# Optimization experiments

Measured on AMD Instinct MI355X. Metric: run time of the kernel, lower is better.

Reference implementation:

```python
import jax, jax.numpy as jnp
import numpy as np

N_NODES = 50000
N_EDGES = 800000


def setup_inputs() -> dict:
    key = jax.random.key(0)
    ks = jax.random.split(key, 8)
    x = jax.random.normal(ks[0], (N_NODES, 128), dtype=jnp.float32)
    edge_index = jax.random.randint(ks[1], (2, N_EDGES), 0, N_NODES, dtype=jnp.int64)
    # Glorot-ish scaled weights (GCNConv uses glorot init)
    W1 = jax.random.normal(ks[2], (128, 128), dtype=jnp.float32) * 0.08
    W2 = jax.random.normal(ks[3], (128, 128), dtype=jnp.float32) * 0.08
    W3 = jax.random.normal(ks[4], (128, 64), dtype=jnp.float32) * 0.08
    b1 = jnp.zeros((128,), jnp.float32)
    b2 = jnp.zeros((128,), jnp.float32)
    b3 = jnp.zeros((64,), jnp.float32)
    return {"x": x, "W1": W1, "b1": b1, "W2": W2, "b2": b2,
            "W3": W3, "b3": b3, "edge_index": edge_index}


def _gcn_layer(x, W, b, src, dst, norm, n):
    # GCNConv: out = D^{-1/2} (A+I) D^{-1/2} (x W) + b
    h = x @ W                                   # [N, F_out]
    msg = h[src] * norm[:, None]                # gather + scale per edge
    agg = jax.ops.segment_sum(msg, dst, num_segments=n)  # scatter-add
    return agg + b


def reference(x, W1, b1, W2, b2, W3, b3, edge_index):
    n = x.shape[0]
    loops = jnp.arange(n, dtype=edge_index.dtype)
    src = jnp.concatenate([edge_index[0], loops])  # add self-loops (PyG default)
    dst = jnp.concatenate([edge_index[1], loops])
    # symmetric normalization from in-degree (incl. self-loops)
    deg = jax.ops.segment_sum(jnp.ones_like(dst, dtype=x.dtype), dst, num_segments=n)
    dis = jnp.where(deg > 0, jax.lax.rsqrt(deg), 0.0)
    norm = dis[src] * dis[dst]                   # [E+N]

    h = jax.nn.relu(_gcn_layer(x, W1, b1, src, dst, norm, n))
    # dropout(p=0.5) is identity in eval mode
    h = jax.nn.relu(_gcn_layer(h, W2, b2, src, dst, norm, n))
    h = _gcn_layer(h, W3, b3, src, dst, norm, n)
    return jax.nn.log_softmax(h, axis=1)
```

## Files before the change

kernel.cpp:

```cpp
#include <hip/hip_runtime.h>
#include <hip/hip_bf16.h>
#include <cstdint>

typedef unsigned int uint32;
typedef unsigned short ushort;
typedef __attribute__((ext_vector_type(8))) short short8;
typedef __attribute__((ext_vector_type(4))) float f32x4;

#define EPB 4096
#define CAP 8192

__device__ inline ushort bf16r(float f) {
    uint32 u = __float_as_uint(f);
    u += 0x7fff + ((u >> 16) & 1);
    return (ushort)(u >> 16);
}
__device__ inline uint32 pack_bf16(float a, float b) {
    return (uint32)bf16r(a) | ((uint32)bf16r(b) << 16);
}
__device__ inline float bf_lo(uint32 w) { return __uint_as_float(w << 16); }
__device__ inline float bf_hi(uint32 w) { return __uint_as_float(w & 0xffff0000u); }


__global__ __launch_bounds__(256) void k_part_prep(
        const int* __restrict__ srcv, const int* __restrict__ dstv,
        int* __restrict__ bcnt, uint64_t* __restrict__ pairs, int e, int nbE,
        const float* __restrict__ W1, const float* __restrict__ W2, const float* __restrict__ W3,
        ushort* __restrict__ Wt1, ushort* __restrict__ Wt2, ushort* __restrict__ Wt3) {
    int bid = blockIdx.x, t = threadIdx.x;
    if (bid >= nbE) {
        int wb = bid - nbE;
        const float* W = wb == 0 ? W1 : (wb == 1 ? W2 : W3);
        ushort* Wt = wb == 0 ? Wt1 : (wb == 1 ? Wt2 : Wt3);
        int F = wb == 2 ? 64 : 128;
        for (int i = t; i < 128 * F; i += 256) {
            int k = i / F, c = i % F;
            Wt[c * 128 + k] = bf16r(W[i]);
        }
        return;
    }
    __shared__ int h[256], base[256], cur[256];
    h[t] = 0; cur[t] = 0;
    __syncthreads();
    int s[EPB / 256], d[EPB / 256];
    int b0 = bid * EPB;
#pragma unroll
    for (int i = 0; i < EPB / 256; ++i) {
        int idx = b0 + i * 256 + t;
        if (idx < e) {
            s[i] = srcv[idx]; d[i] = dstv[idx];
            atomicAdd(&h[d[i] >> 8], 1);
        } else d[i] = -1;
    }
    __syncthreads();
    base[t] = h[t] ? atomicAdd(&bcnt[t], h[t]) : 0;
    __syncthreads();
#pragma unroll
    for (int i = 0; i < EPB / 256; ++i) {
        if (d[i] >= 0) {
            int b = d[i] >> 8;
            int sl = base[b] + atomicAdd(&cur[b], 1);
            if (sl < CAP) {
                uint64_t pk = (uint64_t)(unsigned)s[i] | ((uint64_t)(unsigned)d[i] << 32);
                pairs[(size_t)b * CAP + sl] = pk;
            }
        }
    }
}


__global__ __launch_bounds__(256) void k_bfinish(const uint64_t* __restrict__ pairs,
                                                 const int* __restrict__ bcnt,
                                                 int2* __restrict__ rps, float* __restrict__ dis,
                                                 int* __restrict__ col, int n) {
    __shared__ int c[256], sc[256], cur[256];
    int t = threadIdx.x;
    c[t] = 0; cur[t] = 0;
    __syncthreads();
    int wb = blockIdx.x << 8;
    int e0 = blockIdx.x * CAP;
    int e1 = e0 + min(bcnt[blockIdx.x], CAP);
    for (int i = e0 + t; i < e1; i += 256)
        atomicAdd(&c[(int)(pairs[i] >> 32) - wb], 1);
    __syncthreads();
    int own = c[t];
    sc[t] = own;
    __syncthreads();
    for (int off = 1; off < 256; off <<= 1) {
        int a = (t >= off) ? sc[t - off] : 0;
        __syncthreads();
        sc[t] += a;
        __syncthreads();
    }
    int start = blockIdx.x * CAP + sc[t] - own;
    __syncthreads();
    sc[t] = start;
    int v = wb + t;
    if (v < n) {
        rps[v] = make_int2(start, start + own);
        dis[v] = rsqrtf((float)(own + 1));
    }
    __syncthreads();
    for (int i = e0 + t; i < e1; i += 256) {
        uint64_t p = pairs[i];
        int bl = (int)(p >> 32) - wb;
        int sl = atomicAdd(&cur[bl], 1);
        col[sc[bl] + sl] = (int)(uint32)p;
    }
}


template <int FOUT, bool BF16IN>
__global__ __launch_bounds__(256) void k_gemm_mfma(
        const void* __restrict__ Xv, const ushort* __restrict__ Wt,
        const float* __restrict__ dis, ushort* __restrict__ Yb, int n) {
    constexpr int CT = FOUT / 16;
    int lane = threadIdx.x & 63;
    int wv = threadIdx.x >> 6;
    int r16 = lane & 15, kg = lane >> 4;
    int rowA = blockIdx.x * 64 + wv * 16 + r16;
    int ra = min(rowA, n - 1);
    short8 afr[4];
    if (BF16IN) {
        const ushort* Xb = (const ushort*)Xv;
#pragma unroll
        for (int ks = 0; ks < 4; ++ks)
            afr[ks] = *(const short8*)(Xb + (size_t)ra * 128 + ks * 32 + kg * 8);
    } else {
        const float* Xf = (const float*)Xv;
#pragma unroll
        for (int ks = 0; ks < 4; ++ks) {
            const float* p = Xf + (size_t)ra * 128 + ks * 32 + kg * 8;
            float4 f0 = *(const float4*)p;
            float4 f1 = *(const float4*)(p + 4);
            short8 a;
            a[0] = (short)bf16r(f0.x); a[1] = (short)bf16r(f0.y);
            a[2] = (short)bf16r(f0.z); a[3] = (short)bf16r(f0.w);
            a[4] = (short)bf16r(f1.x); a[5] = (short)bf16r(f1.y);
            a[6] = (short)bf16r(f1.z); a[7] = (short)bf16r(f1.w);
            afr[ks] = a;
        }
    }
    f32x4 acc[CT];
#pragma unroll
    for (int c = 0; c < CT; ++c) acc[c] = (f32x4){0.f, 0.f, 0.f, 0.f};
#pragma unroll
    for (int ks = 0; ks < 4; ++ks) {
#pragma unroll
        for (int c = 0; c < CT; ++c) {
            short8 b = *(const short8*)(Wt + (c * 16 + r16) * 128 + ks * 32 + kg * 8);
            acc[c] = __builtin_amdgcn_mfma_f32_16x16x32_bf16(afr[ks], b, acc[c], 0, 0, 0);
        }
    }
    int rbase = blockIdx.x * 64 + wv * 16 + kg * 4;
#pragma unroll
    for (int j = 0; j < 4; ++j) {
        int row = rbase + j;
        if (row < n) {
            float d = dis[row];
#pragma unroll
            for (int c = 0; c < CT; ++c)
                Yb[(size_t)row * FOUT + c * 16 + r16] = bf16r(acc[c][j] * d);
        }
    }
}


__global__ __launch_bounds__(256) void k_agg_relu128(
        const uint32* __restrict__ hb, const int2* __restrict__ rps,
        const int* __restrict__ col, const float* __restrict__ dis,
        const float* __restrict__ bias, uint32* __restrict__ outb, int n) {
    int wid = threadIdx.x >> 6;
    int lane = threadIdx.x & 63;
    int v = blockIdx.x * 4 + wid;
    if (v >= n) return;
    uint32 mv = hb[(size_t)v * 64 + lane];
    float ax = bf_lo(mv), ay = bf_hi(mv);
    int2 se = rps[v];
    int s = __builtin_amdgcn_readfirstlane(se.x);
    int e = __builtin_amdgcn_readfirstlane(se.y);
    int k = s;
    for (; k + 16 <= e; k += 16) {
        uint32 m[16];
#pragma unroll
        for (int j = 0; j < 16; ++j) {
            int u = col[k + j];
            m[j] = hb[(size_t)u * 64 + lane];
        }
#pragma unroll
        for (int j = 0; j < 16; ++j) { ax += bf_lo(m[j]); ay += bf_hi(m[j]); }
    }
    if (k + 8 <= e) {
        uint32 m[8];
#pragma unroll
        for (int j = 0; j < 8; ++j) m[j] = hb[(size_t)col[k + j] * 64 + lane];
#pragma unroll
        for (int j = 0; j < 8; ++j) { ax += bf_lo(m[j]); ay += bf_hi(m[j]); }
        k += 8;
    }
    if (k + 4 <= e) {
        uint32 m[4];
#pragma unroll
        for (int j = 0; j < 4; ++j) m[j] = hb[(size_t)col[k + j] * 64 + lane];
#pragma unroll
        for (int j = 0; j < 4; ++j) { ax += bf_lo(m[j]); ay += bf_hi(m[j]); }
        k += 4;
    }
    for (; k < e; ++k) {
        uint32 m = hb[(size_t)col[k] * 64 + lane];
        ax += bf_lo(m); ay += bf_hi(m);
    }
    float d = dis[v];
    float2 b = ((const float2*)bias)[lane];
    float ox = fmaxf(d * ax + b.x, 0.f);
    float oy = fmaxf(d * ay + b.y, 0.f);
    __builtin_nontemporal_store(pack_bf16(ox, oy), &outb[(size_t)v * 64 + lane]);
}

__global__ __launch_bounds__(256) void k_agg_lsm64(
        const ushort* __restrict__ hb, const int2* __restrict__ rps,
        const int* __restrict__ col, const float* __restrict__ dis,
        const float* __restrict__ bias, float* __restrict__ out, int n) {
    int wid = threadIdx.x >> 6;
    int lane = threadIdx.x & 63;
    int v = blockIdx.x * 4 + wid;
    if (v >= n) return;
    float acc = __uint_as_float((uint32)hb[(size_t)v * 64 + lane] << 16);
    int2 se = rps[v];
    int s = __builtin_amdgcn_readfirstlane(se.x);
    int e = __builtin_amdgcn_readfirstlane(se.y);
    int k = s;
    for (; k + 16 <= e; k += 16) {
        ushort m[16];
#pragma unroll
        for (int j = 0; j < 16; ++j) m[j] = hb[(size_t)col[k + j] * 64 + lane];
#pragma unroll
        for (int j = 0; j < 16; ++j) acc += __uint_as_float((uint32)m[j] << 16);
    }
    if (k + 8 <= e) {
        ushort m[8];
#pragma unroll
        for (int j = 0; j < 8; ++j) m[j] = hb[(size_t)col[k + j] * 64 + lane];
#pragma unroll
        for (int j = 0; j < 8; ++j) acc += __uint_as_float((uint32)m[j] << 16);
        k += 8;
    }
    for (; k < e; ++k) acc += __uint_as_float((uint32)hb[(size_t)col[k] * 64 + lane] << 16);
    float val = dis[v] * acc + bias[lane];
    float m = val;
    for (int off = 32; off; off >>= 1) m = fmaxf(m, __shfl_xor(m, off, 64));
    float ex = expf(val - m);
    float ss = ex;
    for (int off = 32; off; off >>= 1) ss += __shfl_xor(ss, off, 64);
    __builtin_nontemporal_store(val - m - logf(ss), &out[(size_t)v * 64 + lane]);
}


extern "C" void kernel_launch(void* const* d_in, const int* in_sizes, int n_in,
                              void* d_out, int out_size, void* d_ws, size_t ws_size,
                              hipStream_t stream) {
    const float* x  = (const float*)d_in[0];
    const float* W1 = (const float*)d_in[1];
    const float* b1 = (const float*)d_in[2];
    const float* W2 = (const float*)d_in[3];
    const float* b2 = (const float*)d_in[4];
    const float* W3 = (const float*)d_in[5];
    const float* b3 = (const float*)d_in[6];
    const int*   ei = (const int*)d_in[7];

    const int N = in_sizes[0] / 128;
    const int E = in_sizes[7] / 2;
    const int* srcv = ei;
    const int* dstv = ei + E;
    const int NB  = (N + 255) >> 8;
    const int nbE = (E + EPB - 1) / EPB;

    char* ws = (char*)d_ws;
    size_t off = 0;
    auto alloc = [&](size_t bytes) -> void* {
        void* p = ws + off;
        off += (bytes + 255) & ~(size_t)255;
        return p;
    };
    float*    dis   = (float*)alloc((size_t)N * 4);
    int2*     rps   = (int2*)alloc((size_t)N * 8);
    int*      bcnt  = (int*)alloc((size_t)NB * 4);
    int*      col   = (int*)alloc((size_t)NB * CAP * 4);
    uint64_t* pairs = (uint64_t*)alloc((size_t)NB * CAP * 8);
    ushort*   Wt1   = (ushort*)alloc(128 * 128 * 2);
    ushort*   Wt2   = (ushort*)alloc(128 * 128 * 2);
    ushort*   Wt3   = (ushort*)alloc(64 * 128 * 2);
    ushort*   hsb   = (ushort*)alloc((size_t)N * 128 * 2);
    ushort*   hbX   = (ushort*)alloc((size_t)N * 128 * 2);
    ushort*   hs3   = (ushort*)alloc((size_t)N * 64 * 2);
    float*    outp  = (float*)d_out;

    (void)hipMemsetAsync(bcnt, 0, (size_t)NB * 4, stream);
    k_part_prep<<<nbE + 3, 256, 0, stream>>>(srcv, dstv, bcnt, pairs, E, nbE,
                                             W1, W2, W3, Wt1, Wt2, Wt3);
    k_bfinish<<<NB, 256, 0, stream>>>(pairs, bcnt, rps, dis, col, N);

    int gblk = (N + 63) / 64;
    int ablk = (N + 3) / 4;
    k_gemm_mfma<128, false><<<gblk, 256, 0, stream>>>(x, Wt1, dis, hsb, N);
    k_agg_relu128<<<ablk, 256, 0, stream>>>((const uint32*)hsb, rps, col, dis, b1, (uint32*)hbX, N);
    k_gemm_mfma<128, true><<<gblk, 256, 0, stream>>>(hbX, Wt2, dis, hsb, N);
    k_agg_relu128<<<ablk, 256, 0, stream>>>((const uint32*)hsb, rps, col, dis, b2, (uint32*)hbX, N);
    k_gemm_mfma<64, true><<<gblk, 256, 0, stream>>>(hbX, Wt3, dis, hs3, N);
    k_agg_lsm64<<<ablk, 256, 0, stream>>>(hs3, rps, col, dis, b3, outp, N);
}
```

Measured before the change: 186.0 us.

## Split 128-wide hidden features into two 64-column planes aggregated separately

Hidden feature matrices are stored as two planes of 64 bf16 columns each, and the 128-wide aggregation runs as two passes, one per plane. Each pass gathers 128-byte rows instead of 256-byte rows, so a plane's working set (about 6.4 MB) is more likely to stay in L2/MALL cache during the random neighbor gathers. In exchange the edge list and column indices are read twice, there are extra kernel launches, and each lane now does 16-bit loads.

```diff
diff --git a/kernel.cpp b/kernel.cpp
--- a/kernel.cpp
+++ b/kernel.cpp
@@ -15,11 +15,7 @@
     u += 0x7fff + ((u >> 16) & 1);
     return (ushort)(u >> 16);
 }
-__device__ inline uint32 pack_bf16(float a, float b) {
-    return (uint32)bf16r(a) | ((uint32)bf16r(b) << 16);
-}
-__device__ inline float bf_lo(uint32 w) { return __uint_as_float(w << 16); }
-__device__ inline float bf_hi(uint32 w) { return __uint_as_float(w & 0xffff0000u); }
+__device__ inline float bfu(ushort w) { return __uint_as_float((uint32)w << 16); }
 
 
 __global__ __launch_bounds__(256) void k_part_prep(
@@ -60,10 +56,9 @@
         if (d[i] >= 0) {
             int b = d[i] >> 8;
             int sl = base[b] + atomicAdd(&cur[b], 1);
-            if (sl < CAP) {
-                uint64_t pk = (uint64_t)(unsigned)s[i] | ((uint64_t)(unsigned)d[i] << 32);
-                pairs[(size_t)b * CAP + sl] = pk;
-            }
+            if (sl < CAP)
+                pairs[(size_t)b * CAP + sl] =
+                    (uint64_t)(unsigned)s[i] | ((uint64_t)(unsigned)d[i] << 32);
         }
     }
 }
@@ -110,10 +105,10 @@
 }
 
 
-template <int FOUT, bool BF16IN>
+template <int FOUT, int INMODE>
 __global__ __launch_bounds__(256) void k_gemm_mfma(
         const void* __restrict__ Xv, const ushort* __restrict__ Wt,
-        const float* __restrict__ dis, ushort* __restrict__ Yb, int n) {
+        const float* __restrict__ dis, ushort* __restrict__ Yb, int n, size_t plsz) {
     constexpr int CT = FOUT / 16;
     int lane = threadIdx.x & 63;
     int wv = threadIdx.x >> 6;
@@ -121,11 +116,12 @@
     int rowA = blockIdx.x * 64 + wv * 16 + r16;
     int ra = min(rowA, n - 1);
     short8 afr[4];
-    if (BF16IN) {
+    if (INMODE == 1) {
         const ushort* Xb = (const ushort*)Xv;
 #pragma unroll
         for (int ks = 0; ks < 4; ++ks)
-            afr[ks] = *(const short8*)(Xb + (size_t)ra * 128 + ks * 32 + kg * 8);
+            afr[ks] = *(const short8*)(Xb + (size_t)(ks >> 1) * plsz +
+                                       (size_t)ra * 64 + (ks & 1) * 32 + kg * 8);
     } else {
         const float* Xf = (const float*)Xv;
 #pragma unroll
@@ -159,62 +155,57 @@
         if (row < n) {
             float d = dis[row];
 #pragma unroll
-            for (int c = 0; c < CT; ++c)
-                Yb[(size_t)row * FOUT + c * 16 + r16] = bf16r(acc[c][j] * d);
-        }
-    }
-}
-
-
-__global__ __launch_bounds__(256) void k_agg_relu128(
-        const uint32* __restrict__ hb, const int2* __restrict__ rps,
+            for (int c = 0; c < CT; ++c) {
+                ushort val = bf16r(acc[c][j] * d);
+                if (FOUT == 128)
+                    Yb[(size_t)(c >> 2) * plsz + (size_t)row * 64 + (c & 3) * 16 + r16] = val;
+                else
+                    Yb[(size_t)row * 64 + c * 16 + r16] = val;
+            }
+        }
+    }
+}
+
+
+__global__ __launch_bounds__(256) void k_agg_plane(
+        const ushort* __restrict__ hp, const int2* __restrict__ rps,
         const int* __restrict__ col, const float* __restrict__ dis,
-        const float* __restrict__ bias, uint32* __restrict__ outb, int n) {
+        const float* __restrict__ bias, ushort* __restrict__ outp, int n) {
     int wid = threadIdx.x >> 6;
     int lane = threadIdx.x & 63;
     int v = blockIdx.x * 4 + wid;
     if (v >= n) return;
-    uint32 mv = hb[(size_t)v * 64 + lane];
-    float ax = bf_lo(mv), ay = bf_hi(mv);
+    float ax = bfu(hp[(size_t)v * 64 + lane]);
     int2 se = rps[v];
     int s = __builtin_amdgcn_readfirstlane(se.x);
     int e = __builtin_amdgcn_readfirstlane(se.y);
     int k = s;
     for (; k + 16 <= e; k += 16) {
-        uint32 m[16];
-#pragma unroll
-        for (int j = 0; j < 16; ++j) {
-            int u = col[k + j];
-            m[j] = hb[(size_t)u * 64 + lane];
-        }
-#pragma unroll
-        for (int j = 0; j < 16; ++j) { ax += bf_lo(m[j]); ay += bf_hi(m[j]); }
+        ushort m[16];
+#pragma unroll
+        for (int j = 0; j < 16; ++j) m[j] = hp[(size_t)col[k + j] * 64 + lane];
+#pragma unroll
+        for (int j = 0; j < 16; ++j) ax += bfu(m[j]);
     }
     if (k + 8 <= e) {
-        uint32 m[8];
-#pragma unroll
-        for (int j = 0; j < 8; ++j) m[j] = hb[(size_t)col[k + j] * 64 + lane];
-#pragma unroll
-        for (int j = 0; j < 8; ++j) { ax += bf_lo(m[j]); ay += bf_hi(m[j]); }
+        ushort m[8];
+#pragma unroll
+        for (int j = 0; j < 8; ++j) m[j] = hp[(size_t)col[k + j] * 64 + lane];
+#pragma unroll
+        for (int j = 0; j < 8; ++j) ax += bfu(m[j]);
         k += 8;
     }
     if (k + 4 <= e) {
-        uint32 m[4];
-#pragma unroll
-        for (int j = 0; j < 4; ++j) m[j] = hb[(size_t)col[k + j] * 64 + lane];
-#pragma unroll
-        for (int j = 0; j < 4; ++j) { ax += bf_lo(m[j]); ay += bf_hi(m[j]); }
+        ushort m[4];
+#pragma unroll
+        for (int j = 0; j < 4; ++j) m[j] = hp[(size_t)col[k + j] * 64 + lane];
+#pragma unroll
+        for (int j = 0; j < 4; ++j) ax += bfu(m[j]);
         k += 4;
     }
-    for (; k < e; ++k) {
-        uint32 m = hb[(size_t)col[k] * 64 + lane];
-        ax += bf_lo(m); ay += bf_hi(m);
-    }
-    float d = dis[v];
-    float2 b = ((const float2*)bias)[lane];
-    float ox = fmaxf(d * ax + b.x, 0.f);
-    float oy = fmaxf(d * ay + b.y, 0.f);
-    __builtin_nontemporal_store(pack_bf16(ox, oy), &outb[(size_t)v * 64 + lane]);
+    for (; k < e; ++k) ax += bfu(hp[(size_t)col[k] * 64 + lane]);
+    float ox = fmaxf(dis[v] * ax + bias[lane], 0.f);
+    __builtin_nontemporal_store(bf16r(ox), &outp[(size_t)v * 64 + lane]);
 }
 
 __global__ __launch_bounds__(256) void k_agg_lsm64(
@@ -225,7 +216,7 @@
     int lane = threadIdx.x & 63;
     int v = blockIdx.x * 4 + wid;
     if (v >= n) return;
-    float acc = __uint_as_float((uint32)hb[(size_t)v * 64 + lane] << 16);
+    float acc = bfu(hb[(size_t)v * 64 + lane]);
     int2 se = rps[v];
     int s = __builtin_amdgcn_readfirstlane(se.x);
     int e = __builtin_amdgcn_readfirstlane(se.y);
@@ -235,17 +226,17 @@
 #pragma unroll
         for (int j = 0; j < 16; ++j) m[j] = hb[(size_t)col[k + j] * 64 + lane];
 #pragma unroll
-        for (int j = 0; j < 16; ++j) acc += __uint_as_float((uint32)m[j] << 16);
+        for (int j = 0; j < 16; ++j) acc += bfu(m[j]);
     }
     if (k + 8 <= e) {
         ushort m[8];
 #pragma unroll
         for (int j = 0; j < 8; ++j) m[j] = hb[(size_t)col[k + j] * 64 + lane];
 #pragma unroll
-        for (int j = 0; j < 8; ++j) acc += __uint_as_float((uint32)m[j] << 16);
+        for (int j = 0; j < 8; ++j) acc += bfu(m[j]);
         k += 8;
     }
-    for (; k < e; ++k) acc += __uint_as_float((uint32)hb[(size_t)col[k] * 64 + lane] << 16);
+    for (; k < e; ++k) acc += bfu(hb[(size_t)col[k] * 64 + lane]);
     float val = dis[v] * acc + bias[lane];
     float m = val;
     for (int off = 32; off; off >>= 1) m = fmaxf(m, __shfl_xor(m, off, 64));
@@ -274,6 +265,7 @@
     const int* dstv = ei + E;
     const int NB  = (N + 255) >> 8;
     const int nbE = (E + EPB - 1) / EPB;
+    const size_t PLSZ = (size_t)N * 64;
 
     char* ws = (char*)d_ws;
     size_t off = 0;
@@ -290,9 +282,9 @@
     ushort*   Wt1   = (ushort*)alloc(128 * 128 * 2);
     ushort*   Wt2   = (ushort*)alloc(128 * 128 * 2);
     ushort*   Wt3   = (ushort*)alloc(64 * 128 * 2);
-    ushort*   hsb   = (ushort*)alloc((size_t)N * 128 * 2);
-    ushort*   hbX   = (ushort*)alloc((size_t)N * 128 * 2);
-    ushort*   hs3   = (ushort*)alloc((size_t)N * 64 * 2);
+    ushort*   hsA   = (ushort*)alloc(PLSZ * 2 * 2);
+    ushort*   hbB   = (ushort*)alloc(PLSZ * 2 * 2);
+    ushort*   hs3   = (ushort*)alloc(PLSZ * 2);
     float*    outp  = (float*)d_out;
 
     (void)hipMemsetAsync(bcnt, 0, (size_t)NB * 4, stream);
@@ -302,10 +294,12 @@
 
     int gblk = (N + 63) / 64;
     int ablk = (N + 3) / 4;
-    k_gemm_mfma<128, false><<<gblk, 256, 0, stream>>>(x, Wt1, dis, hsb, N);
-    k_agg_relu128<<<ablk, 256, 0, stream>>>((const uint32*)hsb, rps, col, dis, b1, (uint32*)hbX, N);
-    k_gemm_mfma<128, true><<<gblk, 256, 0, stream>>>(hbX, Wt2, dis, hsb, N);
-    k_agg_relu128<<<ablk, 256, 0, stream>>>((const uint32*)hsb, rps, col, dis, b2, (uint32*)hbX, N);
-    k_gemm_mfma<64, true><<<gblk, 256, 0, stream>>>(hbX, Wt3, dis, hs3, N);
+    k_gemm_mfma<128, 0><<<gblk, 256, 0, stream>>>(x, Wt1, dis, hsA, N, PLSZ);
+    k_agg_plane<<<ablk, 256, 0, stream>>>(hsA,        rps, col, dis, b1,      hbB,        N);
+    k_agg_plane<<<ablk, 256, 0, stream>>>(hsA + PLSZ, rps, col, dis, b1 + 64, hbB + PLSZ, N);
+    k_gemm_mfma<128, 1><<<gblk, 256, 0, stream>>>(hbB, Wt2, dis, hsA, N, PLSZ);
+    k_agg_plane<<<ablk, 256, 0, stream>>>(hsA,        rps, col, dis, b2,      hbB,        N);
+    k_agg_plane<<<ablk, 256, 0, stream>>>(hsA + PLSZ, rps, col, dis, b2 + 64, hbB + PLSZ, N);
+    k_gemm_mfma<64, 1><<<gblk, 256, 0, stream>>>(hbB, Wt3, dis, hs3, N, PLSZ);
     k_agg_lsm64<<<ablk, 256, 0, stream>>>(hs3, rps, col, dis, b3, outp, N);
 }
```

New measurement: 211.1 us. 1.14x slower.

## Split wavefront into sub-groups gathering multiple edges with wider loads

Applied to the files above, without the earlier changes.

The aggregation kernels now split each 64-lane wavefront into 2 groups (128-feature layer) or 4 groups (64-feature layer). Each group processes a different neighbor at the same time and every lane loads 8 bytes instead of 4 or 2. Partial sums are combined with cross-lane shuffles, and the self-loop term and bias are added at the end. This puts more independent row gathers in flight per instruction and widens the memory accesses. The cost is extra shuffles, masked tail iterations, and only half or a quarter of the lanes doing the final stores.

```diff
diff --git a/kernel.cpp b/kernel.cpp
--- a/kernel.cpp
+++ b/kernel.cpp
@@ -60,10 +60,9 @@
         if (d[i] >= 0) {
             int b = d[i] >> 8;
             int sl = base[b] + atomicAdd(&cur[b], 1);
-            if (sl < CAP) {
-                uint64_t pk = (uint64_t)(unsigned)s[i] | ((uint64_t)(unsigned)d[i] << 32);
-                pairs[(size_t)b * CAP + sl] = pk;
-            }
+            if (sl < CAP)
+                pairs[(size_t)b * CAP + sl] =
+                    (uint64_t)(unsigned)s[i] | ((uint64_t)(unsigned)d[i] << 32);
         }
     }
 }
@@ -172,87 +171,137 @@
         const float* __restrict__ bias, uint32* __restrict__ outb, int n) {
     int wid = threadIdx.x >> 6;
     int lane = threadIdx.x & 63;
+    int grp = lane >> 5;
+    int fl  = lane & 31;
     int v = blockIdx.x * 4 + wid;
     if (v >= n) return;
-    uint32 mv = hb[(size_t)v * 64 + lane];
-    float ax = bf_lo(mv), ay = bf_hi(mv);
     int2 se = rps[v];
     int s = __builtin_amdgcn_readfirstlane(se.x);
     int e = __builtin_amdgcn_readfirstlane(se.y);
+    float a0 = 0.f, a1 = 0.f, a2 = 0.f, a3 = 0.f;
     int k = s;
     for (; k + 16 <= e; k += 16) {
-        uint32 m[16];
-#pragma unroll
-        for (int j = 0; j < 16; ++j) {
-            int u = col[k + j];
-            m[j] = hb[(size_t)u * 64 + lane];
-        }
-#pragma unroll
-        for (int j = 0; j < 16; ++j) { ax += bf_lo(m[j]); ay += bf_hi(m[j]); }
+        uint2 m[8];
+#pragma unroll
+        for (int j = 0; j < 8; ++j) {
+            int r = col[k + j * 2 + grp];
+            m[j] = *(const uint2*)(hb + (size_t)r * 64 + fl * 2);
+        }
+#pragma unroll
+        for (int j = 0; j < 8; ++j) {
+            a0 += bf_lo(m[j].x); a1 += bf_hi(m[j].x);
+            a2 += bf_lo(m[j].y); a3 += bf_hi(m[j].y);
+        }
     }
     if (k + 8 <= e) {
-        uint32 m[8];
-#pragma unroll
-        for (int j = 0; j < 8; ++j) m[j] = hb[(size_t)col[k + j] * 64 + lane];
-#pragma unroll
-        for (int j = 0; j < 8; ++j) { ax += bf_lo(m[j]); ay += bf_hi(m[j]); }
+        uint2 m[4];
+#pragma unroll
+        for (int j = 0; j < 4; ++j) {
+            int r = col[k + j * 2 + grp];
+            m[j] = *(const uint2*)(hb + (size_t)r * 64 + fl * 2);
+        }
+#pragma unroll
+        for (int j = 0; j < 4; ++j) {
+            a0 += bf_lo(m[j].x); a1 += bf_hi(m[j].x);
+            a2 += bf_lo(m[j].y); a3 += bf_hi(m[j].y);
+        }
         k += 8;
     }
-    if (k + 4 <= e) {
-        uint32 m[4];
-#pragma unroll
-        for (int j = 0; j < 4; ++j) m[j] = hb[(size_t)col[k + j] * 64 + lane];
-#pragma unroll
-        for (int j = 0; j < 4; ++j) { ax += bf_lo(m[j]); ay += bf_hi(m[j]); }
-        k += 4;
-    }
-    for (; k < e; ++k) {
-        uint32 m = hb[(size_t)col[k] * 64 + lane];
-        ax += bf_lo(m); ay += bf_hi(m);
-    }
+    for (; k < e; k += 2) {
+        int idx = k + grp;
+        bool valid = idx < e;
+        int r = col[min(idx, e - 1)];
+        uint2 m = *(const uint2*)(hb + (size_t)r * 64 + fl * 2);
+        if (valid) {
+            a0 += bf_lo(m.x); a1 += bf_hi(m.x);
+            a2 += bf_lo(m.y); a3 += bf_hi(m.y);
+        }
+    }
+    a0 += __shfl_xor(a0, 32, 64);
+    a1 += __shfl_xor(a1, 32, 64);
+    a2 += __shfl_xor(a2, 32, 64);
+    a3 += __shfl_xor(a3, 32, 64);
+    uint2 mv = *(const uint2*)(hb + (size_t)v * 64 + fl * 2);
+    a0 += bf_lo(mv.x); a1 += bf_hi(mv.x);
+    a2 += bf_lo(mv.y); a3 += bf_hi(mv.y);
     float d = dis[v];
-    float2 b = ((const float2*)bias)[lane];
-    float ox = fmaxf(d * ax + b.x, 0.f);
-    float oy = fmaxf(d * ay + b.y, 0.f);
-    __builtin_nontemporal_store(pack_bf16(ox, oy), &outb[(size_t)v * 64 + lane]);
-}
+    float4 bb = *(const float4*)(bias + fl * 4);
+    float o0 = fmaxf(d * a0 + bb.x, 0.f);
+    float o1 = fmaxf(d * a1 + bb.y, 0.f);
+    float o2 = fmaxf(d * a2 + bb.z, 0.f);
+    float o3 = fmaxf(d * a3 + bb.w, 0.f);
+    if (grp == 0) {
+        uint32* op = outb + (size_t)v * 64 + fl * 2;
+        __builtin_nontemporal_store(pack_bf16(o0, o1), op);
+        __builtin_nontemporal_store(pack_bf16(o2, o3), op + 1);
+    }
+}
+
 
 __global__ __launch_bounds__(256) void k_agg_lsm64(
-        const ushort* __restrict__ hb, const int2* __restrict__ rps,
+        const ushort* __restrict__ hb3, const int2* __restrict__ rps,
         const int* __restrict__ col, const float* __restrict__ dis,
         const float* __restrict__ bias, float* __restrict__ out, int n) {
+    const uint32* hb = (const uint32*)hb3;
     int wid = threadIdx.x >> 6;
     int lane = threadIdx.x & 63;
+    int grp = lane >> 4;
+    int fl  = lane & 15;
     int v = blockIdx.x * 4 + wid;
     if (v >= n) return;
-    float acc = __uint_as_float((uint32)hb[(size_t)v * 64 + lane] << 16);
     int2 se = rps[v];
     int s = __builtin_amdgcn_readfirstlane(se.x);
     int e = __builtin_amdgcn_readfirstlane(se.y);
+    float a0 = 0.f, a1 = 0.f, a2 = 0.f, a3 = 0.f;
     int k = s;
     for (; k + 16 <= e; k += 16) {
-        ushort m[16];
-#pragma unroll
-        for (int j = 0; j < 16; ++j) m[j] = hb[(size_t)col[k + j] * 64 + lane];
-#pragma unroll
-        for (int j = 0; j < 16; ++j) acc += __uint_as_float((uint32)m[j] << 16);
-    }
-    if (k + 8 <= e) {
-        ushort m[8];
-#pragma unroll
-        for (int j = 0; j < 8; ++j) m[j] = hb[(size_t)col[k + j] * 64 + lane];
-#pragma unroll
-        for (int j = 0; j < 8; ++j) acc += __uint_as_float((uint32)m[j] << 16);
-        k += 8;
-    }
-    for (; k < e; ++k) acc += __uint_as_float((uint32)hb[(size_t)col[k] * 64 + lane] << 16);
-    float val = dis[v] * acc + bias[lane];
-    float m = val;
-    for (int off = 32; off; off >>= 1) m = fmaxf(m, __shfl_xor(m, off, 64));
-    float ex = expf(val - m);
-    float ss = ex;
-    for (int off = 32; off; off >>= 1) ss += __shfl_xor(ss, off, 64);
-    __builtin_nontemporal_store(val - m - logf(ss), &out[(size_t)v * 64 + lane]);
+        uint2 m[4];
+#pragma unroll
+        for (int j = 0; j < 4; ++j) {
+            int r = col[k + j * 4 + grp];
+            m[j] = *(const uint2*)(hb + (size_t)r * 32 + fl * 2);
+        }
+#pragma unroll
+        for (int j = 0; j < 4; ++j) {
+            a0 += bf_lo(m[j].x); a1 += bf_hi(m[j].x);
+            a2 += bf_lo(m[j].y); a3 += bf_hi(m[j].y);
+        }
+    }
+    for (; k < e; k += 4) {
+        int idx = k + grp;
+        bool valid = idx < e;
+        int r = col[min(idx, e - 1)];
+        uint2 m = *(const uint2*)(hb + (size_t)r * 32 + fl * 2);
+        if (valid) {
+            a0 += bf_lo(m.x); a1 += bf_hi(m.x);
+            a2 += bf_lo(m.y); a3 += bf_hi(m.y);
+        }
+    }
+    a0 += __shfl_xor(a0, 16, 64); a0 += __shfl_xor(a0, 32, 64);
+    a1 += __shfl_xor(a1, 16, 64); a1 += __shfl_xor(a1, 32, 64);
+    a2 += __shfl_xor(a2, 16, 64); a2 += __shfl_xor(a2, 32, 64);
+    a3 += __shfl_xor(a3, 16, 64); a3 += __shfl_xor(a3, 32, 64);
+    uint2 mv = *(const uint2*)(hb + (size_t)v * 32 + fl * 2);
+    a0 += bf_lo(mv.x); a1 += bf_hi(mv.x);
+    a2 += bf_lo(mv.y); a3 += bf_hi(mv.y);
+    float d = dis[v];
+    float4 bb = *(const float4*)(bias + fl * 4);
+    float v0 = d * a0 + bb.x;
+    float v1 = d * a1 + bb.y;
+    float v2 = d * a2 + bb.z;
+    float v3 = d * a3 + bb.w;
+    float mx = fmaxf(fmaxf(v0, v1), fmaxf(v2, v3));
+    for (int off = 8; off; off >>= 1) mx = fmaxf(mx, __shfl_xor(mx, off, 64));
+    float ss = expf(v0 - mx) + expf(v1 - mx) + expf(v2 - mx) + expf(v3 - mx);
+    for (int off = 8; off; off >>= 1) ss += __shfl_xor(ss, off, 64);
+    float ls = mx + logf(ss);
+    if (grp == 0) {
+        float* op = out + (size_t)v * 64 + fl * 4;
+        __builtin_nontemporal_store(v0 - ls, op);
+        __builtin_nontemporal_store(v1 - ls, op + 1);
+        __builtin_nontemporal_store(v2 - ls, op + 2);
+        __builtin_nontemporal_store(v3 - ls, op + 3);
+    }
 }
 
 
```

After: 196.8 us. 1.06x slower.
